# Kernel tuning notes

Measured on AMD Instinct MI355X. Metric: run time of the kernel, lower is better.

The kernel has to match this reference:

```python
import jax, jax.numpy as jnp
import numpy as np

BN_EPS = 1e-5


def setup_inputs() -> dict:
    key = jax.random.key(0)
    k1, k2, k3, k4, k5 = jax.random.split(key, 5)
    N, C_IN = 400000, 32      # input voxels, input channels
    M, K = 100000, 32         # downsampled voxels, neighbors per voxel
    C_OUT = 64
    voxel_features = jax.random.normal(k1, (N, C_IN), dtype=jnp.float32)
    key_indices = jax.random.randint(k2, (M, K), 0, N, dtype=jnp.int32)
    # key_mask == 1 marks invalid neighbors (original: gather_indices < 0)
    key_mask = jax.random.randint(k3, (M, K), 0, 2, dtype=jnp.int32)
    W = jax.random.normal(k4, (C_OUT, C_IN), dtype=jnp.float32) * (1.0 / np.sqrt(C_IN))
    b = jax.random.normal(k5, (C_OUT,), dtype=jnp.float32) * 0.01
    bn_gamma = jnp.ones((C_OUT,), dtype=jnp.float32)
    bn_beta = jnp.zeros((C_OUT,), dtype=jnp.float32)
    bn_mean = jnp.zeros((C_OUT,), dtype=jnp.float32)
    bn_var = jnp.ones((C_OUT,), dtype=jnp.float32)
    return {"voxel_features": voxel_features, "key_indices": key_indices,
            "key_mask": key_mask, "W": W, "b": b, "bn_gamma": bn_gamma,
            "bn_beta": bn_beta, "bn_mean": bn_mean, "bn_var": bn_var}


def reference(voxel_features, key_indices, key_mask, W, b, bn_gamma, bn_beta, bn_mean, bn_var):
    # grouping_operation: gather neighbor voxel features; invalid (mask==1) -> zeros
    valid = (key_mask == 0)                              # [M, K]
    idx = jnp.maximum(key_indices, 0)                    # clamp negative indices
    gathered = voxel_features[idx]                       # [M, K, C_in]
    gathered = jnp.where(valid[..., None], gathered, 0.0)
    # Conv1d(C_in, C_out, 1): pointwise linear over channels
    proj = jnp.einsum('mkc,oc->mko', gathered, W) + b    # [M, K, C_out]
    # BatchNorm1d (inference: running stats), per output channel
    x = (proj - bn_mean) * (bn_gamma / jnp.sqrt(bn_var + BN_EPS)) + bn_beta
    x = jax.nn.relu(x)
    # down_type == 'max': max over neighbor axis (invalid columns included, as in original)
    new_features = jnp.max(x, axis=1)                    # [M, C_out]
    return new_features
```

## Files before the change

kernel.cpp:

```cpp
#include <hip/hip_runtime.h>
#include <hip/hip_bf16.h>

typedef __bf16 bf16x8 __attribute__((ext_vector_type(8)));
typedef float f32x4 __attribute__((ext_vector_type(4)));
typedef unsigned int u32;
typedef u32 u32x4 __attribute__((ext_vector_type(4)));

#define BN_EPS 1e-5f
#define RB 8

__global__ __launch_bounds__(256) void convert_kernel(
    const float* __restrict__ vf, __bf16* __restrict__ tb, int n8)
{
    int i = blockIdx.x * blockDim.x + threadIdx.x;
    const int stride = gridDim.x * blockDim.x;
    for (; i < n8; i += stride) {
        const f32x4 a = ((const f32x4*)vf)[2 * i];
        const f32x4 b = ((const f32x4*)vf)[2 * i + 1];
        bf16x8 o;
        o[0]=(__bf16)a.x; o[1]=(__bf16)a.y; o[2]=(__bf16)a.z; o[3]=(__bf16)a.w;
        o[4]=(__bf16)b.x; o[5]=(__bf16)b.y; o[6]=(__bf16)b.z; o[7]=(__bf16)b.w;
        ((bf16x8*)tb)[i] = o;
    }
}

__global__ __launch_bounds__(64) void pack_kernel(
    const float* __restrict__ W, const float* __restrict__ bias,
    const float* __restrict__ gamma, const float* __restrict__ beta,
    const float* __restrict__ mean, const float* __restrict__ var,
    __bf16* __restrict__ tb, u32* __restrict__ packB,
    float* __restrict__ SP, float* __restrict__ TP, int N)
{
    const int lane = threadIdx.x;
    const int col = lane & 15, grp = lane >> 4, c0 = grp << 3;
    if (lane < 16) ((u32*)(tb + (size_t)N * 32))[lane] = 0u;
    f32x4 s4, t4;
#pragma unroll
    for (int t = 0; t < 4; ++t) {
        const int o = t * 16 + col;
        const f32x4 w0 = *(const f32x4*)(W + o * 32 + c0);
        const f32x4 w1 = *(const f32x4*)(W + o * 32 + c0 + 4);
        bf16x8 f;
        f[0]=(__bf16)w0.x; f[1]=(__bf16)w0.y; f[2]=(__bf16)w0.z; f[3]=(__bf16)w0.w;
        f[4]=(__bf16)w1.x; f[5]=(__bf16)w1.y; f[6]=(__bf16)w1.z; f[7]=(__bf16)w1.w;
        ((bf16x8*)packB)[t * 64 + lane] = f;
        const float s = gamma[o] * rsqrtf(var[o] + BN_EPS);
        s4[t] = s;
        t4[t] = (bias[o] - mean[o]) * s + beta[o];
    }
    ((f32x4*)SP)[lane] = s4;
    ((f32x4*)TP)[lane] = t4;
}

__global__ __launch_bounds__(256, 4) void down_bf16(
    const __bf16* __restrict__ tb,
    const int*   __restrict__ kidx,
    const int*   __restrict__ kmask,
    const u32*   __restrict__ packB,
    const float* __restrict__ SP,
    const float* __restrict__ TP,
    float* __restrict__ out,
    int M, int N)
{
    const int lane = threadIdx.x & 63;
    const int col  = lane & 15;
    const int grp  = lane >> 4;
    const int c0   = grp << 3;

    const int wave_id = blockIdx.x * (blockDim.x >> 6) + (threadIdx.x >> 6);
    const int m0 = wave_id * RB;
    if (m0 >= M) return;

    const int elim  = M * 32 - 1;
    const int ebase = m0 * 32 + lane;
    int ci[4], cm[4];
#pragma unroll
    for (int i = 0; i < 4; ++i) {
        int e = ebase + i * 64; e = e < elim ? e : elim;
        ci[i] = __builtin_nontemporal_load(kidx + e);
    }
#pragma unroll
    for (int i = 0; i < 4; ++i) {
        int e = ebase + i * 64; e = e < elim ? e : elim;
        cm[i] = __builtin_nontemporal_load(kmask + e);
    }

    bf16x8 bfrag[4];
#pragma unroll
    for (int t = 0; t < 4; ++t)
        bfrag[t] = ((const bf16x8*)packB)[t * 64 + lane];
    const f32x4 Sv = ((const f32x4*)SP)[lane];
    const f32x4 Tv = ((const f32x4*)TP)[lane];

    int fid[RB][2];
#pragma unroll
    for (int r = 0; r < RB; ++r) {
#pragma unroll
        for (int kt = 0; kt < 2; ++kt) {
            const int srcl = ((r & 1) << 5) + (kt << 4) + col;
            int idv = __shfl(ci[r >> 1], srcl, 64);
            int mkv = __shfl(cm[r >> 1], srcl, 64);
            idv = idv < 0 ? 0 : idv;
            fid[r][kt] = (mkv == 0) ? idv : N;
        }
    }

    u32x4 g[RB][2];
#pragma unroll
    for (int r = 0; r < RB; ++r)
#pragma unroll
        for (int kt = 0; kt < 2; ++kt)
            g[r][kt] = *(const u32x4*)(tb + (size_t)fid[r][kt] * 32 + c0);

    const f32x4 zero4 = {0.f, 0.f, 0.f, 0.f};
#pragma unroll
    for (int r = 0; r < RB; ++r) {
        const int m = m0 + r;
        const bf16x8 a0 = __builtin_bit_cast(bf16x8, g[r][0]);
        const bf16x8 a1 = __builtin_bit_cast(bf16x8, g[r][1]);
        float myout = 0.0f;
#pragma unroll
        for (int t = 0; t < 4; ++t) {
            f32x4 d0 = __builtin_amdgcn_mfma_f32_16x16x32_bf16(a0, bfrag[t], zero4, 0, 0, 0);
            f32x4 d1 = __builtin_amdgcn_mfma_f32_16x16x32_bf16(a1, bfrag[t], zero4, 0, 0, 0);
            float v = 0.0f;
#pragma unroll
            for (int q = 0; q < 4; ++q) {
                v = fmaxf(v, d0[q] * Sv[t] + Tv[t]);
                v = fmaxf(v, d1[q] * Sv[t] + Tv[t]);
            }
            v = fmaxf(v, __shfl_xor(v, 16));
            v = fmaxf(v, __shfl_xor(v, 32));
            if (grp == t) myout = v;
        }
        if (m < M) __builtin_nontemporal_store(myout, out + (size_t)m * 64 + lane);
    }
}

__global__ __launch_bounds__(256, 4) void down_fp32(
    const float* __restrict__ vf, const int* __restrict__ kidx,
    const int* __restrict__ kmask, const float* __restrict__ W,
    const float* __restrict__ bias, const float* __restrict__ gamma,
    const float* __restrict__ beta, const float* __restrict__ mean,
    const float* __restrict__ var, float* __restrict__ out, int M)
{
    const int lane = threadIdx.x & 63;
    const int col  = lane & 15;
    const int grp  = lane >> 4;
    const int c0   = grp << 3;
    const int waves_per_block = blockDim.x >> 6;
    const int wave_id     = blockIdx.x * waves_per_block + (threadIdx.x >> 6);
    const int total_waves = gridDim.x * waves_per_block;

    bf16x8 bfrag[4];
    float S[4], T[4];
#pragma unroll
    for (int t = 0; t < 4; ++t) {
        const int o = t * 16 + col;
        const f32x4 w0 = *(const f32x4*)(W + o * 32 + c0);
        const f32x4 w1 = *(const f32x4*)(W + o * 32 + c0 + 4);
        bf16x8 f;
        f[0]=(__bf16)w0.x; f[1]=(__bf16)w0.y; f[2]=(__bf16)w0.z; f[3]=(__bf16)w0.w;
        f[4]=(__bf16)w1.x; f[5]=(__bf16)w1.y; f[6]=(__bf16)w1.z; f[7]=(__bf16)w1.w;
        bfrag[t] = f;
        const float s = gamma[o] * rsqrtf(var[o] + BN_EPS);
        S[t] = s;
        T[t] = (bias[o] - mean[o]) * s + beta[o];
    }
    const f32x4 zero4 = {0.f, 0.f, 0.f, 0.f};
    for (int m = wave_id; m < M; m += total_waves) {
        const int* idxp = kidx  + (size_t)m * 32;
        const int* mskp = kmask + (size_t)m * 32;
        bf16x8 afrag[2];
#pragma unroll
        for (int kt = 0; kt < 2; ++kt) {
            const int k = kt * 16 + col;
            int id = idxp[k]; id = id < 0 ? 0 : id;
            const float sel = (mskp[k] == 0) ? 1.0f : 0.0f;
            const float* src = vf + (size_t)id * 32 + c0;
            const f32x4 g0 = *(const f32x4*)(src);
            const f32x4 g1 = *(const f32x4*)(src + 4);
            bf16x8 a;
            a[0]=(__bf16)(g0.x*sel); a[1]=(__bf16)(g0.y*sel);
            a[2]=(__bf16)(g0.z*sel); a[3]=(__bf16)(g0.w*sel);
            a[4]=(__bf16)(g1.x*sel); a[5]=(__bf16)(g1.y*sel);
            a[6]=(__bf16)(g1.z*sel); a[7]=(__bf16)(g1.w*sel);
            afrag[kt] = a;
        }
        float myout = 0.0f;
#pragma unroll
        for (int t = 0; t < 4; ++t) {
            f32x4 d0 = __builtin_amdgcn_mfma_f32_16x16x32_bf16(afrag[0], bfrag[t], zero4, 0, 0, 0);
            f32x4 d1 = __builtin_amdgcn_mfma_f32_16x16x32_bf16(afrag[1], bfrag[t], zero4, 0, 0, 0);
            float v = 0.0f;
#pragma unroll
            for (int q = 0; q < 4; ++q) {
                v = fmaxf(v, d0[q] * S[t] + T[t]);
                v = fmaxf(v, d1[q] * S[t] + T[t]);
            }
            v = fmaxf(v, __shfl_xor(v, 16));
            v = fmaxf(v, __shfl_xor(v, 32));
            if (grp == t) myout = v;
        }
        out[(size_t)m * 64 + lane] = myout;
    }
}

extern "C" void kernel_launch(void* const* d_in, const int* in_sizes, int n_in,
                              void* d_out, int out_size, void* d_ws, size_t ws_size,
                              hipStream_t stream) {
    const float* vf    = (const float*)d_in[0];
    const int*   kidx  = (const int*)  d_in[1];
    const int*   kmask = (const int*)  d_in[2];
    const float* W     = (const float*)d_in[3];
    const float* bias  = (const float*)d_in[4];
    const float* gamma = (const float*)d_in[5];
    const float* beta  = (const float*)d_in[6];
    const float* mean  = (const float*)d_in[7];
    const float* var   = (const float*)d_in[8];
    float* out = (float*)d_out;

    const int NC = in_sizes[0];
    const int N  = NC / 32;
    const int M  = in_sizes[1] / 32;

    const size_t tbBytes = ((size_t)N + 1) * 32 * sizeof(__bf16);
    const size_t packOff = tbBytes;
    const size_t need    = packOff + 4096 + 1024 + 1024;

    if (ws_size >= need) {
        __bf16* tb    = (__bf16*)d_ws;
        u32*    packB = (u32*)  ((char*)d_ws + packOff);
        float*  SP    = (float*)((char*)d_ws + packOff + 4096);
        float*  TP    = (float*)((char*)d_ws + packOff + 4096 + 1024);

        pack_kernel<<<1, 64, 0, stream>>>(W, bias, gamma, beta, mean, var,
                                          tb, packB, SP, TP, N);
        convert_kernel<<<2048, 256, 0, stream>>>(vf, tb, NC / 8);

        const int rows_per_block = (256 / 64) * RB;
        const int blocks = (M + rows_per_block - 1) / rows_per_block;
        down_bf16<<<blocks, 256, 0, stream>>>(tb, kidx, kmask, packB, SP, TP,
                                              out, M, N);
    } else {
        down_fp32<<<2048, 256, 0, stream>>>(vf, kidx, kmask, W, bias, gamma,
                                            beta, mean, var, out, M);
    }
}
```

Baseline: 58.23 us.

## Convert gather kernel to persistent grid-stride loop with double-buffered prefetch

```diff
diff --git a/kernel.cpp b/kernel.cpp
--- a/kernel.cpp
+++ b/kernel.cpp
@@ -7,7 +7,9 @@
 typedef u32 u32x4 __attribute__((ext_vector_type(4)));
 
 #define BN_EPS 1e-5f
-#define RB 8
+#define RB 4
+#define NBLK 1024
+#define NTHR 256
 
 __global__ __launch_bounds__(256) void convert_kernel(
     const float* __restrict__ vf, __bf16* __restrict__ tb, int n8)
@@ -52,6 +54,71 @@
     ((f32x4*)TP)[lane] = t4;
 }
 
+__device__ __forceinline__ void loadIdx(const int* __restrict__ kidx,
+                                        const int* __restrict__ kmask,
+                                        int mb, int lane, int elim,
+                                        int ci[2], int cm[2])
+{
+#pragma unroll
+    for (int i = 0; i < 2; ++i) {
+        int e = mb * 32 + lane + i * 64; e = e < elim ? e : elim;
+        ci[i] = __builtin_nontemporal_load(kidx + e);
+    }
+#pragma unroll
+    for (int i = 0; i < 2; ++i) {
+        int e = mb * 32 + lane + i * 64; e = e < elim ? e : elim;
+        cm[i] = __builtin_nontemporal_load(kmask + e);
+    }
+}
+
+__device__ __forceinline__ void issueGathers(const __bf16* __restrict__ tb, int N,
+                                             const int ci[2], const int cm[2],
+                                             int col, int c0, u32x4 g[RB][2])
+{
+#pragma unroll
+    for (int r = 0; r < RB; ++r)
+#pragma unroll
+        for (int kt = 0; kt < 2; ++kt) {
+            const int srcl = ((r & 1) << 5) + (kt << 4) + col;
+            int idv = __shfl(ci[r >> 1], srcl, 64);
+            int mkv = __shfl(cm[r >> 1], srcl, 64);
+            idv = idv < 0 ? 0 : idv;
+            idv = (mkv == 0) ? idv : N;
+            g[r][kt] = *(const u32x4*)(tb + (size_t)idv * 32 + c0);
+        }
+}
+
+__device__ __forceinline__ void computeStore(const u32x4 g[RB][2], int mb, int M,
+                                             int lane, int grp,
+                                             const bf16x8 bfrag[4],
+                                             f32x4 Sv, f32x4 Tv,
+                                             float* __restrict__ out)
+{
+    const f32x4 zero4 = {0.f, 0.f, 0.f, 0.f};
+#pragma unroll
+    for (int r = 0; r < RB; ++r) {
+        const int m = mb + r;
+        const bf16x8 a0 = __builtin_bit_cast(bf16x8, g[r][0]);
+        const bf16x8 a1 = __builtin_bit_cast(bf16x8, g[r][1]);
+        float myout = 0.0f;
+#pragma unroll
+        for (int t = 0; t < 4; ++t) {
+            f32x4 d0 = __builtin_amdgcn_mfma_f32_16x16x32_bf16(a0, bfrag[t], zero4, 0, 0, 0);
+            f32x4 d1 = __builtin_amdgcn_mfma_f32_16x16x32_bf16(a1, bfrag[t], zero4, 0, 0, 0);
+            float v = 0.0f;
+#pragma unroll
+            for (int q = 0; q < 4; ++q) {
+                v = fmaxf(v, d0[q] * Sv[t] + Tv[t]);
+                v = fmaxf(v, d1[q] * Sv[t] + Tv[t]);
+            }
+            v = fmaxf(v, __shfl_xor(v, 16));
+            v = fmaxf(v, __shfl_xor(v, 32));
+            if (grp == t) myout = v;
+        }
+        if (m < M) __builtin_nontemporal_store(myout, out + (size_t)m * 64 + lane);
+    }
+}
+
 __global__ __launch_bounds__(256, 4) void down_bf16(
     const __bf16* __restrict__ tb,
     const int*   __restrict__ kidx,
@@ -67,23 +134,13 @@
     const int grp  = lane >> 4;
     const int c0   = grp << 3;
 
-    const int wave_id = blockIdx.x * (blockDim.x >> 6) + (threadIdx.x >> 6);
+    const int wave_id = blockIdx.x * (NTHR >> 6) + (threadIdx.x >> 6);
+    const int nwaves  = NBLK * (NTHR >> 6);
+    const int stride  = nwaves * RB;
+    const int elim    = M * 32 - 1;
+
     const int m0 = wave_id * RB;
     if (m0 >= M) return;
-
-    const int elim  = M * 32 - 1;
-    const int ebase = m0 * 32 + lane;
-    int ci[4], cm[4];
-#pragma unroll
-    for (int i = 0; i < 4; ++i) {
-        int e = ebase + i * 64; e = e < elim ? e : elim;
-        ci[i] = __builtin_nontemporal_load(kidx + e);
-    }
-#pragma unroll
-    for (int i = 0; i < 4; ++i) {
-        int e = ebase + i * 64; e = e < elim ? e : elim;
-        cm[i] = __builtin_nontemporal_load(kmask + e);
-    }
 
     bf16x8 bfrag[4];
 #pragma unroll
@@ -92,48 +149,26 @@
     const f32x4 Sv = ((const f32x4*)SP)[lane];
     const f32x4 Tv = ((const f32x4*)TP)[lane];
 
-    int fid[RB][2];
-#pragma unroll
-    for (int r = 0; r < RB; ++r) {
-#pragma unroll
-        for (int kt = 0; kt < 2; ++kt) {
-            const int srcl = ((r & 1) << 5) + (kt << 4) + col;
-            int idv = __shfl(ci[r >> 1], srcl, 64);
-            int mkv = __shfl(cm[r >> 1], srcl, 64);
-            idv = idv < 0 ? 0 : idv;
-            fid[r][kt] = (mkv == 0) ? idv : N;
-        }
-    }
-
-    u32x4 g[RB][2];
-#pragma unroll
-    for (int r = 0; r < RB; ++r)
-#pragma unroll
-        for (int kt = 0; kt < 2; ++kt)
-            g[r][kt] = *(const u32x4*)(tb + (size_t)fid[r][kt] * 32 + c0);
-
-    const f32x4 zero4 = {0.f, 0.f, 0.f, 0.f};
-#pragma unroll
-    for (int r = 0; r < RB; ++r) {
-        const int m = m0 + r;
-        const bf16x8 a0 = __builtin_bit_cast(bf16x8, g[r][0]);
-        const bf16x8 a1 = __builtin_bit_cast(bf16x8, g[r][1]);
-        float myout = 0.0f;
-#pragma unroll
-        for (int t = 0; t < 4; ++t) {
-            f32x4 d0 = __builtin_amdgcn_mfma_f32_16x16x32_bf16(a0, bfrag[t], zero4, 0, 0, 0);
-            f32x4 d1 = __builtin_amdgcn_mfma_f32_16x16x32_bf16(a1, bfrag[t], zero4, 0, 0, 0);
-            float v = 0.0f;
-#pragma unroll
-            for (int q = 0; q < 4; ++q) {
-                v = fmaxf(v, d0[q] * Sv[t] + Tv[t]);
-                v = fmaxf(v, d1[q] * Sv[t] + Tv[t]);
-            }
-            v = fmaxf(v, __shfl_xor(v, 16));
-            v = fmaxf(v, __shfl_xor(v, 32));
-            if (grp == t) myout = v;
-        }
-        if (m < M) __builtin_nontemporal_store(myout, out + (size_t)m * 64 + lane);
+    int ciA[2], cmA[2], ciB[2], cmB[2];
+    u32x4 gA[RB][2], gB[RB][2];
+
+    loadIdx(kidx, kmask, m0,          lane, elim, ciA, cmA);
+    loadIdx(kidx, kmask, m0 + stride, lane, elim, ciB, cmB);
+    issueGathers(tb, N, ciA, cmA, col, c0, gA);
+
+    int mc = m0;
+    while (true) {
+        issueGathers(tb, N, ciB, cmB, col, c0, gB);
+        loadIdx(kidx, kmask, mc + 2 * stride, lane, elim, ciA, cmA);
+        computeStore(gA, mc, M, lane, grp, bfrag, Sv, Tv, out);
+        mc += stride;
+        if (mc >= M) break;
+
+        issueGathers(tb, N, ciA, cmA, col, c0, gA);
+        loadIdx(kidx, kmask, mc + 2 * stride, lane, elim, ciB, cmB);
+        computeStore(gB, mc, M, lane, grp, bfrag, Sv, Tv, out);
+        mc += stride;
+        if (mc >= M) break;
     }
 }
 
@@ -237,11 +272,8 @@
         pack_kernel<<<1, 64, 0, stream>>>(W, bias, gamma, beta, mean, var,
                                           tb, packB, SP, TP, N);
         convert_kernel<<<2048, 256, 0, stream>>>(vf, tb, NC / 8);
-
-        const int rows_per_block = (256 / 64) * RB;
-        const int blocks = (M + rows_per_block - 1) / rows_per_block;
-        down_bf16<<<blocks, 256, 0, stream>>>(tb, kidx, kmask, packB, SP, TP,
-                                              out, M, N);
+        down_bf16<<<NBLK, NTHR, 0, stream>>>(tb, kidx, kmask, packB, SP, TP,
+                                             out, M, N);
     } else {
         down_fp32<<<2048, 256, 0, stream>>>(vf, kidx, kmask, W, bias, gamma,
                                             beta, mean, var, out, M);
```

After: 59.22 us. Within noise of the previous version (+1.7%).
